# Kernel tuning notes

Measured on AMD Instinct MI355X. Metric: run time of the kernel, lower is better.

Reference implementation:

```python
import jax, jax.numpy as jnp
import numpy as np

B, H, W, C = 4, 256, 256, 192
WS, SHIFT, NH = 8, 4, 6
HD = C // NH            # 32
N = WS * WS             # 64 tokens per window
NW = (H // WS) * (W // WS)  # 1024 windows per image
HIDDEN = 4 * C
SCALE = HD ** -0.5
EPS = 1e-5


def _swin_attn_mask():
    # standard Swin shifted-window mask: 0 where tokens share a region, -100 otherwise
    img = np.zeros((H, W), np.float32)
    cnt = 0
    for hs in (slice(0, -WS), slice(-WS, -SHIFT), slice(-SHIFT, None)):
        for ws_ in (slice(0, -WS), slice(-WS, -SHIFT), slice(-SHIFT, None)):
            img[hs, ws_] = cnt
            cnt += 1
    mw = img.reshape(H // WS, WS, W // WS, WS).transpose(0, 2, 1, 3).reshape(-1, N)
    diff = mw[:, None, :] - mw[:, :, None]
    return np.where(diff != 0, -100.0, 0.0).astype(np.float32)  # (NW, N, N)


def _rel_pos_index():
    coords = np.stack(np.meshgrid(np.arange(WS), np.arange(WS), indexing='ij')).reshape(2, -1)
    rel = (coords[:, :, None] - coords[:, None, :]).transpose(1, 2, 0)
    rel[:, :, 0] += WS - 1
    rel[:, :, 1] += WS - 1
    rel[:, :, 0] *= 2 * WS - 1
    return rel.sum(-1).astype(np.int32)  # (N, N)


def setup_inputs() -> dict:
    key = jax.random.key(0)
    ks = jax.random.split(key, 12)
    s = 0.02
    x = jax.random.normal(ks[0], (B, H * W, C), jnp.float32)
    mask_matrix = jnp.asarray(_swin_attn_mask())
    rel_idx = jnp.asarray(_rel_pos_index())
    return {
        'x': x,
        'mask_matrix': mask_matrix,
        'rel_idx': rel_idx,
        'qkv_w': jax.random.normal(ks[1], (3 * C, C), jnp.float32) * s,
        'qkv_b': jnp.zeros((3 * C,), jnp.float32),
        'proj_w': jax.random.normal(ks[2], (C, C), jnp.float32) * s,
        'proj_b': jnp.zeros((C,), jnp.float32),
        'rpb_table': jax.random.normal(ks[3], ((2 * WS - 1) * (2 * WS - 1), NH), jnp.float32) * s,
        'norm1_g': jnp.ones((C,), jnp.float32),
        'norm1_b': jnp.zeros((C,), jnp.float32),
        'norm2_g': jnp.ones((C,), jnp.float32),
        'norm2_b': jnp.zeros((C,), jnp.float32),
        'fc1_w': jax.random.normal(ks[4], (HIDDEN, C), jnp.float32) * s,
        'fc1_b': jnp.zeros((HIDDEN,), jnp.float32),
        'fc2_w': jax.random.normal(ks[5], (C, HIDDEN), jnp.float32) * s,
        'fc2_b': jnp.zeros((C,), jnp.float32),
    }


def _layernorm(y, g, b):
    mu = y.mean(-1, keepdims=True)
    var = ((y - mu) ** 2).mean(-1, keepdims=True)
    return (y - mu) * jax.lax.rsqrt(var + EPS) * g + b


def reference(x, mask_matrix, rel_idx, qkv_w, qkv_b, proj_w, proj_b, rpb_table,
              norm1_g, norm1_b, norm2_g, norm2_b, fc1_w, fc1_b, fc2_w, fc2_b):
    shortcut = x
    xi = x.reshape(B, H, W, C)
    # cyclic shift (H,W already multiples of WS -> no padding needed)
    xs = jnp.roll(xi, (-SHIFT, -SHIFT), (1, 2))
    # window partition -> (B*NW, N, C)
    win = xs.reshape(B, H // WS, WS, W // WS, WS, C).transpose(0, 1, 3, 2, 4, 5).reshape(-1, N, C)
    B_ = win.shape[0]
    qkv = (win @ qkv_w.T + qkv_b).reshape(B_, N, 3, NH, HD).transpose(2, 0, 3, 1, 4)
    q, k, v = qkv[0] * SCALE, qkv[1], qkv[2]        # (B_, NH, N, HD)
    attn = jnp.einsum('bhnd,bhmd->bhnm', q, k)       # (B_, NH, N, N)
    rpb = rpb_table[rel_idx.reshape(-1)].reshape(N, N, NH).transpose(2, 0, 1)
    attn = attn + rpb[None]
    nWm = mask_matrix.shape[0]
    attn = attn.reshape(B_ // nWm, nWm, NH, N, N) + mask_matrix[None, :, None]
    attn = jax.nn.softmax(attn.reshape(B_, NH, N, N), axis=-1)
    out = jnp.einsum('bhnm,bhmd->bhnd', attn, v).transpose(0, 2, 1, 3).reshape(B_, N, C)
    out = out @ proj_w.T + proj_b
    # window reverse + reverse shift
    xr = out.reshape(B, H // WS, W // WS, WS, WS, C).transpose(0, 1, 3, 2, 4, 5).reshape(B, H, W, C)
    xr = jnp.roll(xr, (SHIFT, SHIFT), (1, 2)).reshape(B, H * W, C)
    x1 = shortcut + _layernorm(xr, norm1_g, norm1_b)  # post-norm residual as in source
    h = jax.nn.gelu(x1 @ fc1_w.T + fc1_b, approximate=False)
    m = h @ fc2_w.T + fc2_b
    return x1 + _layernorm(m, norm2_g, norm2_b)
```

## Files before the change

### kernel.cpp

```cpp
#include <hip/hip_runtime.h>
#include <hip/hip_bf16.h>
#include <math.h>

typedef unsigned short u16;
typedef unsigned int   u32;
typedef __attribute__((ext_vector_type(8))) short bf16x8;
typedef __attribute__((ext_vector_type(4))) float f32x4;

__device__ __forceinline__ u16 f2bf(float f){
  u32 u = __float_as_uint(f);
  u += 0x7fffu + ((u>>16)&1u);
  return (u16)(u>>16);
}
__device__ __forceinline__ u32 pack2(float a, float b){
  return (u32)f2bf(a) | ((u32)f2bf(b)<<16);
}
__device__ __forceinline__ float2 LDF2(const float* p){ return *(const float2*)p; }
__device__ __forceinline__ float gelu_f(float v){
  float t = __expf(1.5957691216057308f * fmaf(0.044715f*v, v*v, v));
  return v - v/(t + 1.0f);
}

#define ST_U32(p,v) (*(u32*)(p) = (v))
#define MFMA16(a,b,c) __builtin_amdgcn_mfma_f32_16x16x32_bf16((a),(b),(c),0,0,0)

__device__ __forceinline__ bf16x8 ldsfrag(const u16* p){ return *(const bf16x8*)p; }
__device__ __forceinline__ bf16x8 gfrag(const u16* p){ return *(const bf16x8*)p; }

constexpr float SCALE_Q = 0.17677669529663687f;
constexpr float LN_EPS  = 1e-5f;

#define NQKV 110592
#define NPRJ 36864
#define NFC  147456

__global__ void k_prep(const float* __restrict__ qkv_w, const float* __restrict__ proj_w,
                       const float* __restrict__ fc1_w, const float* __restrict__ fc2_w,
                       const float* __restrict__ rpb, const int* __restrict__ relidx,
                       u16* __restrict__ qkv_bf, u16* __restrict__ proj_bf,
                       u16* __restrict__ fc1_bf, u16* __restrict__ fc2_bf,
                       float* __restrict__ rpbm)
{
  int stride = gridDim.x * blockDim.x;
  int t = blockIdx.x * blockDim.x + threadIdx.x;
  for (int i = t; i < NQKV; i += stride) qkv_bf[i] = f2bf(qkv_w[i]);
  for (int i = t; i < NPRJ; i += stride) proj_bf[i] = f2bf(proj_w[i]);
  for (int i = t; i < NFC;  i += stride) fc1_bf[i]  = f2bf(fc1_w[i]);
  for (int i = t; i < NFC;  i += stride) fc2_bf[i]  = f2bf(fc2_w[i]);
  for (int i = t; i < 6*4096; i += stride){
    int h = i >> 12, ij = i & 4095;
    rpbm[i] = rpb[relidx[ij]*6 + h];
  }
}

__global__ __launch_bounds__(256, 3) void k_attn(
    const float* __restrict__ x, const float* __restrict__ mask,
    const float* __restrict__ rpbm, const u16* __restrict__ qkv_bf,
    const float* __restrict__ qkv_b, const u16* __restrict__ proj_bf,
    const float* __restrict__ proj_b, const float* __restrict__ n1g,
    const float* __restrict__ n1b, float* __restrict__ x1)
{
  __shared__ __align__(16) u16 xw[64*200];
  __shared__ __align__(16) u16 qkvh[64*72];
  __shared__ __align__(16) u16 vT[32*72];
  __shared__ __align__(16) u16 prb[64*72];
  __shared__ __align__(16) u16 outh[64*40];
  float* lnred = (float*)outh;

  const int tid  = threadIdx.x;
  const int wave = tid >> 6, lane = tid & 63;
  const int kg   = lane >> 4, l15 = lane & 15;
  const int wi = blockIdx.x;
  const int b  = wi >> 10, wm = wi & 1023;
  const int wh = wm >> 5,  ww = wm & 31;
  const size_t imgbase = (size_t)b * (256*256*192);

  for (int s = tid; s < 64*96; s += 256){
    int t = s / 96, c2 = s - t*96;
    int i = t >> 3, j = t & 7;
    int h0 = ((wh<<3) + i + 4) & 255;
    int w0 = ((ww<<3) + j + 4) & 255;
    float2 v = LDF2(x + imgbase + (size_t)(h0*256 + w0)*192 + c2*2);
    ST_U32(xw + t*200 + c2*2, pack2(v.x, v.y));
  }

  f32x4 pj[4][3];
  #pragma unroll
  for (int mt = 0; mt < 4; ++mt)
    #pragma unroll
    for (int nt = 0; nt < 3; ++nt){
      float bv = proj_b[wave*48 + nt*16 + l15];
      pj[mt][nt] = {bv, bv, bv, bv};
    }
  __syncthreads();

  #pragma unroll 1
  for (int h = 0; h < 6; ++h){
    f32x4 qa[6];
    #pragma unroll
    for (int nt = 0; nt < 6; ++nt){
      float bv = qkv_b[(nt>>1)*192 + h*32 + (nt&1)*16 + l15];
      qa[nt] = {bv, bv, bv, bv};
    }
    #pragma unroll 2
    for (int kt = 0; kt < 6; ++kt){
      bf16x8 af = ldsfrag(xw + (wave*16 + l15)*200 + kt*32 + kg*8);
      #pragma unroll
      for (int nt = 0; nt < 6; ++nt){
        bf16x8 bfr = gfrag(qkv_bf + ((nt>>1)*192 + h*32 + (nt&1)*16 + l15)*192 + kt*32 + kg*8);
        qa[nt] = MFMA16(af, bfr, qa[nt]);
      }
    }
    #pragma unroll
    for (int nt = 0; nt < 2; ++nt)
      #pragma unroll
      for (int r = 0; r < 4; ++r)
        qkvh[(wave*16 + kg*4 + r)*72 + nt*16 + l15] = f2bf(qa[nt][r]*SCALE_Q);
    #pragma unroll
    for (int nt = 2; nt < 4; ++nt)
      #pragma unroll
      for (int r = 0; r < 4; ++r)
        qkvh[(wave*16 + kg*4 + r)*72 + 32 + (nt-2)*16 + l15] = f2bf(qa[nt][r]);
    #pragma unroll
    for (int nt = 4; nt < 6; ++nt)
      #pragma unroll
      for (int r = 0; r < 4; ++r)
        vT[((nt-4)*16 + l15)*72 + wave*16 + kg*4 + r] = f2bf(qa[nt][r]);
    __syncthreads();

    f32x4 at[4];
    {
      const f32x4 z = {0.f, 0.f, 0.f, 0.f};
      bf16x8 qf = ldsfrag(qkvh + (wave*16 + l15)*72 + kg*8);
      #pragma unroll
      for (int nt = 0; nt < 4; ++nt){
        bf16x8 kf = ldsfrag(qkvh + (nt*16 + l15)*72 + 32 + kg*8);
        at[nt] = MFMA16(qf, kf, z);
      }
    }
    {
      const float* rb = rpbm + h*4096;
      const float* mb = mask + (size_t)wm*4096;
      #pragma unroll
      for (int nt = 0; nt < 4; ++nt)
        #pragma unroll
        for (int r = 0; r < 4; ++r){
          int idx = (wave*16 + kg*4 + r)*64 + nt*16 + l15;
          at[nt][r] += rb[idx] + mb[idx];
        }
    }
    #pragma unroll
    for (int r = 0; r < 4; ++r){
      float m0 = fmaxf(fmaxf(at[0][r], at[1][r]), fmaxf(at[2][r], at[3][r]));
      #pragma unroll
      for (int mk = 1; mk < 16; mk <<= 1) m0 = fmaxf(m0, __shfl_xor(m0, mk));
      float s = 0.f;
      #pragma unroll
      for (int nt = 0; nt < 4; ++nt){ at[nt][r] = __expf(at[nt][r] - m0); s += at[nt][r]; }
      #pragma unroll
      for (int mk = 1; mk < 16; mk <<= 1) s += __shfl_xor(s, mk);
      float inv = 1.0f / s;
      #pragma unroll
      for (int nt = 0; nt < 4; ++nt) at[nt][r] *= inv;
    }
    #pragma unroll
    for (int nt = 0; nt < 4; ++nt)
      #pragma unroll
      for (int r = 0; r < 4; ++r)
        prb[(wave*16 + kg*4 + r)*72 + nt*16 + l15] = f2bf(at[nt][r]);

    {
      f32x4 ov[2] = {{0,0,0,0},{0,0,0,0}};
      #pragma unroll
      for (int kt = 0; kt < 2; ++kt){
        bf16x8 pf = ldsfrag(prb + (wave*16 + l15)*72 + kt*32 + kg*8);
        #pragma unroll
        for (int nt = 0; nt < 2; ++nt){
          bf16x8 vf = ldsfrag(vT + (nt*16 + l15)*72 + kt*32 + kg*8);
          ov[nt] = MFMA16(pf, vf, ov[nt]);
        }
      }
      #pragma unroll
      for (int nt = 0; nt < 2; ++nt)
        #pragma unroll
        for (int r = 0; r < 4; ++r)
          outh[(wave*16 + kg*4 + r)*40 + nt*16 + l15] = f2bf(ov[nt][r]);
    }
    __syncthreads();

    {
      bf16x8 pw[3];
      #pragma unroll
      for (int nt = 0; nt < 3; ++nt)
        pw[nt] = gfrag(proj_bf + (wave*48 + nt*16 + l15)*192 + h*32 + kg*8);
      #pragma unroll
      for (int mt = 0; mt < 4; ++mt){
        bf16x8 af = ldsfrag(outh + (mt*16 + l15)*40 + kg*8);
        #pragma unroll
        for (int nt = 0; nt < 3; ++nt)
          pj[mt][nt] = MFMA16(af, pw[nt], pj[mt][nt]);
      }
    }
    __syncthreads();
  }

  float gv[3], bv2[3];
  #pragma unroll
  for (int nt = 0; nt < 3; ++nt){
    int c = wave*48 + nt*16 + l15;
    gv[nt] = n1g[c]; bv2[nt] = n1b[c];
  }
  #pragma unroll
  for (int mt = 0; mt < 4; ++mt)
    #pragma unroll
    for (int r = 0; r < 4; ++r){
      float s1 = pj[mt][0][r] + pj[mt][1][r] + pj[mt][2][r];
      float s2 = pj[mt][0][r]*pj[mt][0][r] + pj[mt][1][r]*pj[mt][1][r] + pj[mt][2][r]*pj[mt][2][r];
      #pragma unroll
      for (int mk = 1; mk < 16; mk <<= 1){ s1 += __shfl_xor(s1, mk); s2 += __shfl_xor(s2, mk); }
      if (l15 == 0){
        int t = mt*16 + kg*4 + r;
        lnred[t*8 + wave*2]     = s1;
        lnred[t*8 + wave*2 + 1] = s2;
      }
    }
  __syncthreads();
  #pragma unroll
  for (int mt = 0; mt < 4; ++mt)
    #pragma unroll 1
    for (int r = 0; r < 4; ++r){
      int t = mt*16 + kg*4 + r;
      float a1 = lnred[t*8+0] + lnred[t*8+2] + lnred[t*8+4] + lnred[t*8+6];
      float a2 = lnred[t*8+1] + lnred[t*8+3] + lnred[t*8+5] + lnred[t*8+7];
      float mu = a1 * (1.f/192.f);
      float rs = rsqrtf(a2 * (1.f/192.f) - mu*mu + LN_EPS);
      int i = t >> 3, j = t & 7;
      int h0 = ((wh<<3) + i + 4) & 255, w0 = ((ww<<3) + j + 4) & 255;
      size_t base = imgbase + (size_t)(h0*256 + w0)*192;
      #pragma unroll
      for (int nt = 0; nt < 3; ++nt){
        int c = wave*48 + nt*16 + l15;
        x1[base + c] = x[base + c] + (pj[mt][nt][r] - mu)*rs*gv[nt] + bv2[nt];
      }
    }
}

__global__ __launch_bounds__(256, 3) void k_mlp(
    float* xio, const u16* __restrict__ fc1_bf,
    const float* __restrict__ fc1_b, const u16* __restrict__ fc2_bf,
    const float* __restrict__ fc2_b, const float* __restrict__ n2g,
    const float* __restrict__ n2b)
{
  __shared__ __align__(16) u16 xt[64*200];
  __shared__ __align__(16) u16 hl[64*200];
  __shared__ float lnred[64*8];

  const int tid  = threadIdx.x;
  const int wave = tid >> 6, lane = tid & 63;
  const int kg   = lane >> 4, l15 = lane & 15;
  const size_t t0 = (size_t)blockIdx.x * 64;

  for (int s = tid; s < 64*96; s += 256){
    int t = s / 96, c2 = s - t*96;
    float2 v = LDF2(xio + (t0 + t)*192 + c2*2);
    ST_U32(xt + t*200 + c2*2, pack2(v.x, v.y));
  }
  f32x4 m2[4][3];
  #pragma unroll
  for (int mt = 0; mt < 4; ++mt)
    #pragma unroll
    for (int nt = 0; nt < 3; ++nt){
      float bv = fc2_b[wave*48 + nt*16 + l15];
      m2[mt][nt] = {bv, bv, bv, bv};
    }
  __syncthreads();

  #pragma unroll 1
  for (int c = 0; c < 4; ++c){
    f32x4 a1[4][3];
    #pragma unroll
    for (int mt = 0; mt < 4; ++mt)
      #pragma unroll
      for (int nt = 0; nt < 3; ++nt){
        float bv = fc1_b[c*192 + wave*48 + nt*16 + l15];
        a1[mt][nt] = {bv, bv, bv, bv};
      }
    #pragma unroll 2
    for (int kt = 0; kt < 6; ++kt){
      bf16x8 af[4];
      #pragma unroll
      for (int mt = 0; mt < 4; ++mt)
        af[mt] = ldsfrag(xt + (mt*16 + l15)*200 + kt*32 + kg*8);
      #pragma unroll
      for (int nt = 0; nt < 3; ++nt){
        bf16x8 bfr = gfrag(fc1_bf + (size_t)(c*192 + wave*48 + nt*16 + l15)*192 + kt*32 + kg*8);
        #pragma unroll
        for (int mt = 0; mt < 4; ++mt)
          a1[mt][nt] = MFMA16(af[mt], bfr, a1[mt][nt]);
      }
    }
    #pragma unroll
    for (int mt = 0; mt < 4; ++mt)
      #pragma unroll
      for (int nt = 0; nt < 3; ++nt)
        #pragma unroll
        for (int r = 0; r < 4; ++r)
          hl[(mt*16 + kg*4 + r)*200 + wave*48 + nt*16 + l15] = f2bf(gelu_f(a1[mt][nt][r]));
    __syncthreads();

    #pragma unroll 2
    for (int kt = 0; kt < 6; ++kt){
      bf16x8 af[4];
      #pragma unroll
      for (int mt = 0; mt < 4; ++mt)
        af[mt] = ldsfrag(hl + (mt*16 + l15)*200 + kt*32 + kg*8);
      #pragma unroll
      for (int nt = 0; nt < 3; ++nt){
        bf16x8 bfr = gfrag(fc2_bf + (size_t)(wave*48 + nt*16 + l15)*768 + c*192 + kt*32 + kg*8);
        #pragma unroll
        for (int mt = 0; mt < 4; ++mt)
          m2[mt][nt] = MFMA16(af[mt], bfr, m2[mt][nt]);
      }
    }
    __syncthreads();
  }

  float gv[3], bv2[3];
  #pragma unroll
  for (int nt = 0; nt < 3; ++nt){
    int cc = wave*48 + nt*16 + l15;
    gv[nt] = n2g[cc]; bv2[nt] = n2b[cc];
  }
  #pragma unroll
  for (int mt = 0; mt < 4; ++mt)
    #pragma unroll
    for (int r = 0; r < 4; ++r){
      float s1 = m2[mt][0][r] + m2[mt][1][r] + m2[mt][2][r];
      float s2 = m2[mt][0][r]*m2[mt][0][r] + m2[mt][1][r]*m2[mt][1][r] + m2[mt][2][r]*m2[mt][2][r];
      #pragma unroll
      for (int mk = 1; mk < 16; mk <<= 1){ s1 += __shfl_xor(s1, mk); s2 += __shfl_xor(s2, mk); }
      if (l15 == 0){
        int t = mt*16 + kg*4 + r;
        lnred[t*8 + wave*2]     = s1;
        lnred[t*8 + wave*2 + 1] = s2;
      }
    }
  __syncthreads();
  #pragma unroll
  for (int mt = 0; mt < 4; ++mt)
    #pragma unroll 1
    for (int r = 0; r < 4; ++r){
      int t = mt*16 + kg*4 + r;
      float a1s = lnred[t*8+0] + lnred[t*8+2] + lnred[t*8+4] + lnred[t*8+6];
      float a2s = lnred[t*8+1] + lnred[t*8+3] + lnred[t*8+5] + lnred[t*8+7];
      float mu = a1s * (1.f/192.f);
      float rs = rsqrtf(a2s * (1.f/192.f) - mu*mu + LN_EPS);
      size_t base = (t0 + t)*192;
      #pragma unroll
      for (int nt = 0; nt < 3; ++nt){
        int cc = wave*48 + nt*16 + l15;
        xio[base + cc] = xio[base + cc] + (m2[mt][nt][r] - mu)*rs*gv[nt] + bv2[nt];
      }
    }
}

extern "C" void kernel_launch(void* const* d_in, const int* in_sizes, int n_in,
                              void* d_out, int out_size, void* d_ws, size_t ws_size,
                              hipStream_t stream)
{
  const float* x      = (const float*)d_in[0];
  const float* mask   = (const float*)d_in[1];
  const int*   relidx = (const int*)d_in[2];
  const float* qkv_w  = (const float*)d_in[3];
  const float* qkv_b  = (const float*)d_in[4];
  const float* proj_w = (const float*)d_in[5];
  const float* proj_b = (const float*)d_in[6];
  const float* rpb    = (const float*)d_in[7];
  const float* n1g    = (const float*)d_in[8];
  const float* n1b    = (const float*)d_in[9];
  const float* n2g    = (const float*)d_in[10];
  const float* n2b    = (const float*)d_in[11];
  const float* fc1_w  = (const float*)d_in[12];
  const float* fc1_b  = (const float*)d_in[13];
  const float* fc2_w  = (const float*)d_in[14];
  const float* fc2_b  = (const float*)d_in[15];
  float* xio = (float*)d_out;

  u16* qkv_bf  = (u16*)d_ws;
  u16* proj_bf = qkv_bf + NQKV;
  u16* fc1_bf  = proj_bf + NPRJ;
  u16* fc2_bf  = fc1_bf + NFC;
  float* rpbm  = (float*)(fc2_bf + NFC);

  k_prep<<<dim3(512), dim3(256), 0, stream>>>(qkv_w, proj_w, fc1_w, fc2_w,
      rpb, relidx, qkv_bf, proj_bf, fc1_bf, fc2_bf, rpbm);
  k_attn<<<dim3(4096), dim3(256), 0, stream>>>(x, mask, rpbm, qkv_bf, qkv_b,
      proj_bf, proj_b, n1g, n1b, xio);
  k_mlp<<<dim3(4096), dim3(256), 0, stream>>>(xio, fc1_bf, fc1_b, fc2_bf, fc2_b,
      n2g, n2b);
}
```

Baseline: 1.037 ms.

## Split fused window attention into QKV projection and attention kernels via workspace

When the workspace is large enough, the fused attention kernel is split in two. The first kernel computes QKV per window and writes Q (pre-scaled), K and transposed V as bf16 to global memory. The second kernel reads them directly into MFMA fragments, applies a transposed bias+mask layout for vectorized loads, does softmax, PV, projection and LayerNorm. This lowers LDS use and register pressure to raise occupancy, at the cost of about 300MB extra global traffic for the Q/K/V round trip.

New measurement: 939.8 us, median of 4. 9.4% less time.

```diff
diff --git a/kernel.cpp b/kernel.cpp
--- a/kernel.cpp
+++ b/kernel.cpp
@@ -33,13 +33,18 @@
 #define NQKV 110592
 #define NPRJ 36864
 #define NFC  147456
+#define QKV_SLAB 50331648ull
+#define WS_WEIGHTS_B 884736ull
+#define WS_RPBM_B    98304ull
+#define WS_SPLIT_HDR (WS_WEIGHTS_B + 2*WS_RPBM_B)
+#define WS_SPLIT_NEED (WS_SPLIT_HDR + 3ull*QKV_SLAB*2ull)
 
 __global__ void k_prep(const float* __restrict__ qkv_w, const float* __restrict__ proj_w,
                        const float* __restrict__ fc1_w, const float* __restrict__ fc2_w,
                        const float* __restrict__ rpb, const int* __restrict__ relidx,
                        u16* __restrict__ qkv_bf, u16* __restrict__ proj_bf,
                        u16* __restrict__ fc1_bf, u16* __restrict__ fc2_bf,
-                       float* __restrict__ rpbm)
+                       float* __restrict__ rpbm, float* __restrict__ rpbmT, int mode)
 {
   int stride = gridDim.x * blockDim.x;
   int t = blockIdx.x * blockDim.x + threadIdx.x;
@@ -51,6 +56,235 @@
     int h = i >> 12, ij = i & 4095;
     rpbm[i] = rpb[relidx[ij]*6 + h];
   }
+  if (mode){
+    for (int i = t; i < 6*4096; i += stride){
+      int h = i >> 12, ij = i & 4095;
+      int col = ij >> 6, row = ij & 63;
+      rpbmT[i] = rpb[relidx[row*64 + col]*6 + h];
+    }
+  }
+}
+
+__global__ __launch_bounds__(256, 4) void k_qkv(
+    const float* __restrict__ x, const u16* __restrict__ qkv_bf,
+    const float* __restrict__ qkv_b,
+    u16* __restrict__ Qg, u16* __restrict__ Kg, u16* __restrict__ VTg)
+{
+  __shared__ __align__(16) u16 xw[64*200];
+  const int tid = threadIdx.x, wave = tid >> 6, lane = tid & 63;
+  const int kg = lane >> 4, l15 = lane & 15;
+  const int wi = blockIdx.x, b = wi >> 10, wm = wi & 1023;
+  const int wh = wm >> 5, ww = wm & 31;
+  const size_t imgbase = (size_t)b * (256*256*192);
+
+  for (int s = tid; s < 64*96; s += 256){
+    int t = s / 96, c2 = s - t*96;
+    int i = t >> 3, j = t & 7;
+    int h0 = ((wh<<3) + i + 4) & 255;
+    int w0 = ((ww<<3) + j + 4) & 255;
+    float2 v = LDF2(x + imgbase + (size_t)(h0*256 + w0)*192 + c2*2);
+    ST_U32(xw + t*200 + c2*2, pack2(v.x, v.y));
+  }
+  __syncthreads();
+
+  const size_t wbase = (size_t)wi * 12288;
+  #pragma unroll 1
+  for (int batch = 0; batch < 3; ++batch){
+    const int col0 = wave*144 + batch*48;
+    f32x4 a[4][3];
+    #pragma unroll
+    for (int j = 0; j < 3; ++j){
+      float bv = qkv_b[col0 + j*16 + l15];
+      #pragma unroll
+      for (int mt = 0; mt < 4; ++mt) a[mt][j] = {bv, bv, bv, bv};
+    }
+    #pragma unroll 2
+    for (int kt = 0; kt < 6; ++kt){
+      bf16x8 af[4];
+      #pragma unroll
+      for (int mt = 0; mt < 4; ++mt)
+        af[mt] = ldsfrag(xw + (mt*16 + l15)*200 + kt*32 + kg*8);
+      #pragma unroll
+      for (int j = 0; j < 3; ++j){
+        bf16x8 bfr = gfrag(qkv_bf + (col0 + j*16 + l15)*192 + kt*32 + kg*8);
+        #pragma unroll
+        for (int mt = 0; mt < 4; ++mt)
+          a[mt][j] = MFMA16(af[mt], bfr, a[mt][j]);
+      }
+    }
+    #pragma unroll
+    for (int j = 0; j < 3; ++j){
+      int colg = col0 + j*16 + l15;
+      if (colg < 192){
+        #pragma unroll
+        for (int mt = 0; mt < 4; ++mt)
+          #pragma unroll
+          for (int r = 0; r < 4; ++r)
+            Qg[wbase + (size_t)(mt*16 + kg*4 + r)*192 + colg] = f2bf(a[mt][j][r]*SCALE_Q);
+      } else if (colg < 384){
+        #pragma unroll
+        for (int mt = 0; mt < 4; ++mt)
+          #pragma unroll
+          for (int r = 0; r < 4; ++r)
+            Kg[wbase + (size_t)(mt*16 + kg*4 + r)*192 + (colg - 192)] = f2bf(a[mt][j][r]);
+      } else {
+        #pragma unroll
+        for (int mt = 0; mt < 4; ++mt){
+          ushort4 pk = { f2bf(a[mt][j][0]), f2bf(a[mt][j][1]),
+                         f2bf(a[mt][j][2]), f2bf(a[mt][j][3]) };
+          *(ushort4*)(VTg + wbase + (size_t)(colg - 384)*64 + mt*16 + kg*4) = pk;
+        }
+      }
+    }
+  }
+}
+
+__global__ __launch_bounds__(256, 4) void k_attn2(
+    const float* __restrict__ x, const float* __restrict__ mask,
+    const float* __restrict__ rpbmT,
+    const u16* __restrict__ Qg, const u16* __restrict__ Kg,
+    const u16* __restrict__ VTg,
+    const u16* __restrict__ proj_bf, const float* __restrict__ proj_b,
+    const float* __restrict__ n1g, const float* __restrict__ n1b,
+    float* __restrict__ x1)
+{
+  __shared__ __align__(16) u16 prb[64*72];
+  __shared__ __align__(16) u16 obuf[64*200];
+  __shared__ float lnred[64*8];
+
+  const int tid = threadIdx.x, wave = tid >> 6, lane = tid & 63;
+  const int kg = lane >> 4, l15 = lane & 15;
+  const int wi = blockIdx.x, b = wi >> 10, wm = wi & 1023;
+  const int wh = wm >> 5, ww = wm & 31;
+  const size_t imgbase = (size_t)b * (256*256*192);
+  const size_t wbase = (size_t)wi * 12288;
+
+  f32x4 pj[4][3];
+  #pragma unroll
+  for (int mt = 0; mt < 4; ++mt)
+    #pragma unroll
+    for (int nt = 0; nt < 3; ++nt){
+      float bv = proj_b[wave*48 + nt*16 + l15];
+      pj[mt][nt] = {bv, bv, bv, bv};
+    }
+
+  #pragma unroll 1
+  for (int h = 0; h < 6; ++h){
+    const f32x4 z = {0.f, 0.f, 0.f, 0.f};
+    bf16x8 qf = gfrag(Qg + wbase + (size_t)(wave*16 + l15)*192 + h*32 + kg*8);
+    f32x4 at[4];
+    #pragma unroll
+    for (int nt = 0; nt < 4; ++nt){
+      bf16x8 kf = gfrag(Kg + wbase + (size_t)(nt*16 + l15)*192 + h*32 + kg*8);
+      at[nt] = MFMA16(qf, kf, z);
+    }
+    {
+      const float* rb = rpbmT + h*4096;
+      const float* mb = mask + (size_t)wm*4096;
+      #pragma unroll
+      for (int nt = 0; nt < 4; ++nt){
+        int cidx = (nt*16 + l15)*64 + wave*16 + kg*4;
+        float4 r4 = *(const float4*)(rb + cidx);
+        float4 m4 = *(const float4*)(mb + cidx);
+        at[nt][0] += r4.x + m4.x;
+        at[nt][1] += r4.y + m4.y;
+        at[nt][2] += r4.z + m4.z;
+        at[nt][3] += r4.w + m4.w;
+      }
+    }
+    #pragma unroll
+    for (int r = 0; r < 4; ++r){
+      float m0 = fmaxf(fmaxf(at[0][r], at[1][r]), fmaxf(at[2][r], at[3][r]));
+      #pragma unroll
+      for (int mk = 1; mk < 16; mk <<= 1) m0 = fmaxf(m0, __shfl_xor(m0, mk));
+      float s = 0.f;
+      #pragma unroll
+      for (int nt = 0; nt < 4; ++nt){ at[nt][r] = __expf(at[nt][r] - m0); s += at[nt][r]; }
+      #pragma unroll
+      for (int mk = 1; mk < 16; mk <<= 1) s += __shfl_xor(s, mk);
+      float inv = 1.0f / s;
+      #pragma unroll
+      for (int nt = 0; nt < 4; ++nt) at[nt][r] *= inv;
+    }
+    #pragma unroll
+    for (int nt = 0; nt < 4; ++nt)
+      #pragma unroll
+      for (int r = 0; r < 4; ++r)
+        prb[(wave*16 + kg*4 + r)*72 + nt*16 + l15] = f2bf(at[nt][r]);
+    {
+      f32x4 ov[2] = {z, z};
+      #pragma unroll
+      for (int kt = 0; kt < 2; ++kt){
+        bf16x8 pf = ldsfrag(prb + (wave*16 + l15)*72 + kt*32 + kg*8);
+        #pragma unroll
+        for (int d = 0; d < 2; ++d){
+          bf16x8 vf = gfrag(VTg + wbase + (size_t)(h*32 + d*16 + l15)*64 + kt*32 + kg*8);
+          ov[d] = MFMA16(pf, vf, ov[d]);
+        }
+      }
+      #pragma unroll
+      for (int d = 0; d < 2; ++d)
+        #pragma unroll
+        for (int r = 0; r < 4; ++r)
+          obuf[(wave*16 + kg*4 + r)*200 + h*32 + d*16 + l15] = f2bf(ov[d][r]);
+    }
+  }
+  __syncthreads();
+
+  #pragma unroll 2
+  for (int kt = 0; kt < 6; ++kt){
+    bf16x8 af[4];
+    #pragma unroll
+    for (int mt = 0; mt < 4; ++mt)
+      af[mt] = ldsfrag(obuf + (mt*16 + l15)*200 + kt*32 + kg*8);
+    #pragma unroll
+    for (int nt = 0; nt < 3; ++nt){
+      bf16x8 bfr = gfrag(proj_bf + (wave*48 + nt*16 + l15)*192 + kt*32 + kg*8);
+      #pragma unroll
+      for (int mt = 0; mt < 4; ++mt)
+        pj[mt][nt] = MFMA16(af[mt], bfr, pj[mt][nt]);
+    }
+  }
+
+  float gv[3], bv2[3];
+  #pragma unroll
+  for (int nt = 0; nt < 3; ++nt){
+    int c = wave*48 + nt*16 + l15;
+    gv[nt] = n1g[c]; bv2[nt] = n1b[c];
+  }
+  #pragma unroll
+  for (int mt = 0; mt < 4; ++mt)
+    #pragma unroll
+    for (int r = 0; r < 4; ++r){
+      float s1 = pj[mt][0][r] + pj[mt][1][r] + pj[mt][2][r];
+      float s2 = pj[mt][0][r]*pj[mt][0][r] + pj[mt][1][r]*pj[mt][1][r] + pj[mt][2][r]*pj[mt][2][r];
+      #pragma unroll
+      for (int mk = 1; mk < 16; mk <<= 1){ s1 += __shfl_xor(s1, mk); s2 += __shfl_xor(s2, mk); }
+      if (l15 == 0){
+        int t = mt*16 + kg*4 + r;
+        lnred[t*8 + wave*2]     = s1;
+        lnred[t*8 + wave*2 + 1] = s2;
+      }
+    }
+  __syncthreads();
+  #pragma unroll
+  for (int mt = 0; mt < 4; ++mt)
+    #pragma unroll 1
+    for (int r = 0; r < 4; ++r){
+      int t = mt*16 + kg*4 + r;
+      float a1 = lnred[t*8+0] + lnred[t*8+2] + lnred[t*8+4] + lnred[t*8+6];
+      float a2 = lnred[t*8+1] + lnred[t*8+3] + lnred[t*8+5] + lnred[t*8+7];
+      float mu = a1 * (1.f/192.f);
+      float rs = rsqrtf(a2 * (1.f/192.f) - mu*mu + LN_EPS);
+      int i = t >> 3, j = t & 7;
+      int h0 = ((wh<<3) + i + 4) & 255, w0 = ((ww<<3) + j + 4) & 255;
+      size_t base = imgbase + (size_t)(h0*256 + w0)*192;
+      #pragma unroll
+      for (int nt = 0; nt < 3; ++nt){
+        int c = wave*48 + nt*16 + l15;
+        x1[base + c] = x[base + c] + (pj[mt][nt][r] - mu)*rs*gv[nt] + bv2[nt];
+      }
+    }
 }
 
 __global__ __launch_bounds__(256, 3) void k_attn(
@@ -391,11 +625,23 @@
   u16* fc1_bf  = proj_bf + NPRJ;
   u16* fc2_bf  = fc1_bf + NFC;
   float* rpbm  = (float*)(fc2_bf + NFC);
+  float* rpbmT = rpbm + 6*4096;
+  u16* Qg = (u16*)((char*)d_ws + WS_SPLIT_HDR);
+  u16* Kg = Qg + QKV_SLAB;
+  u16* VTg = Kg + QKV_SLAB;
+
+  const int split = (ws_size >= WS_SPLIT_NEED) ? 1 : 0;
 
   k_prep<<<dim3(512), dim3(256), 0, stream>>>(qkv_w, proj_w, fc1_w, fc2_w,
-      rpb, relidx, qkv_bf, proj_bf, fc1_bf, fc2_bf, rpbm);
-  k_attn<<<dim3(4096), dim3(256), 0, stream>>>(x, mask, rpbm, qkv_bf, qkv_b,
-      proj_bf, proj_b, n1g, n1b, xio);
+      rpb, relidx, qkv_bf, proj_bf, fc1_bf, fc2_bf, rpbm, rpbmT, split);
+  if (split){
+    k_qkv<<<dim3(4096), dim3(256), 0, stream>>>(x, qkv_bf, qkv_b, Qg, Kg, VTg);
+    k_attn2<<<dim3(4096), dim3(256), 0, stream>>>(x, mask, rpbmT, Qg, Kg, VTg,
+        proj_bf, proj_b, n1g, n1b, xio);
+  } else {
+    k_attn<<<dim3(4096), dim3(256), 0, stream>>>(x, mask, rpbm, qkv_bf, qkv_b,
+        proj_bf, proj_b, n1g, n1b, xio);
+  }
   k_mlp<<<dim3(4096), dim3(256), 0, stream>>>(xio, fc1_bf, fc1_b, fc2_bf, fc2_b,
       n2g, n2b);
 }
```
